# Performance work log

Measured on AMD Instinct MI355X. Metric: run time of the kernel, lower is better.

Reference implementation:

```python
import jax, jax.numpy as jnp
import numpy as np

N_NODES = 100000
N_EDGES = 1600000
IN_C, HID_C, OUT_C = 128, 128, 64


def setup_inputs() -> dict:
    key = jax.random.key(0)
    ks = jax.random.split(key, 5)
    x = jax.random.normal(ks[0], (N_NODES, IN_C), dtype=jnp.float32)
    edge_index = jax.random.randint(ks[1], (2, N_EDGES), 0, N_NODES, dtype=jnp.int32)
    W1 = jax.random.normal(ks[2], (IN_C, HID_C), dtype=jnp.float32) * (1.0 / np.sqrt(IN_C))
    W2 = jax.random.normal(ks[3], (HID_C, HID_C), dtype=jnp.float32) * (1.0 / np.sqrt(HID_C))
    W3 = jax.random.normal(ks[4], (HID_C, OUT_C), dtype=jnp.float32) * (1.0 / np.sqrt(HID_C))
    b1 = jnp.zeros((HID_C,), jnp.float32)
    b2 = jnp.zeros((HID_C,), jnp.float32)
    b3 = jnp.zeros((OUT_C,), jnp.float32)
    return {"x": x, "edge_index": edge_index, "W1": W1, "b1": b1,
            "W2": W2, "b2": b2, "W3": W3, "b3": b3}


def _gcn_norm(edge_index, num_nodes):
    # PyG gcn_norm: add self-loops, symmetric normalization D^-1/2 A D^-1/2
    loops = jnp.arange(num_nodes, dtype=edge_index.dtype)
    row = jnp.concatenate([edge_index[0], loops])  # source nodes
    col = jnp.concatenate([edge_index[1], loops])  # target nodes
    ones = jnp.ones(row.shape[0], jnp.float32)
    deg = jax.ops.segment_sum(ones, col, num_segments=num_nodes)
    dinv = jnp.where(deg > 0, jax.lax.rsqrt(deg), 0.0)
    norm = dinv[row] * dinv[col]  # [E + N]
    return row, col, norm


def _gcn_conv(h, row, col, norm, W, b, num_nodes):
    h = h @ W                                   # [N, out] dense transform first
    msg = h[row] * norm[:, None]                # gather + scale, [E+N, out]
    out = jax.ops.segment_sum(msg, col, num_segments=num_nodes)  # scatter-add
    return out + b


def reference(x, edge_index, W1, b1, W2, b2, W3, b3):
    n = x.shape[0]
    row, col, norm = _gcn_norm(edge_index, n)
    h = jax.nn.relu(_gcn_conv(x, row, col, norm, W1, b1, n))
    h = jax.nn.relu(_gcn_conv(h, row, col, norm, W2, b2, n))
    h = _gcn_conv(h, row, col, norm, W3, b3, n)
    return h
```

## Files before the change

kernel.cpp:

```cpp
#include <hip/hip_runtime.h>
#include <hip/hip_fp16.h>


#define K_DIM 128
#define CHUNK 8192
#define NBMAX 1024

typedef _Float16 f16x8 __attribute__((ext_vector_type(8)));
typedef float f32x4 __attribute__((ext_vector_type(4)));


__global__ __launch_bounds__(256) void hist_pass(const int* __restrict__ col, int E,
                                                 int NB, int B1, int* __restrict__ histG) {
    __shared__ int h[NBMAX];
    const int tid = threadIdx.x;
    for (int i = tid; i < NB; i += 256) h[i] = 0;
    __syncthreads();
    const int base = blockIdx.x * CHUNK;
    const int end = min(base + CHUNK, E);
    for (int e = base + tid; e < end; e += 256) atomicAdd(&h[col[e] >> 7], 1);
    __syncthreads();
    for (int i = tid; i < NB; i += 256) histG[(size_t)i * B1 + blockIdx.x] = h[i];
}

__global__ __launch_bounds__(256) void scan_blocks(int* __restrict__ data, int n,
                                                   int* __restrict__ bsum) {
    __shared__ int sh[256];
    const int tid = threadIdx.x;
    const int base = blockIdx.x * 1024;
    int v[4];
    int sum = 0;
#pragma unroll
    for (int j = 0; j < 4; ++j) {
        int i = base + tid * 4 + j;
        v[j] = (i < n) ? data[i] : 0;
        sum += v[j];
    }
    sh[tid] = sum;
    __syncthreads();
#pragma unroll
    for (int off = 1; off < 256; off <<= 1) {
        int t = (tid >= off) ? sh[tid - off] : 0;
        __syncthreads();
        sh[tid] += t;
        __syncthreads();
    }
    int run = (tid > 0) ? sh[tid - 1] : 0;
#pragma unroll
    for (int j = 0; j < 4; ++j) {
        int i = base + tid * 4 + j;
        if (i < n) data[i] = run;
        run += v[j];
    }
    if (tid == 255) bsum[blockIdx.x] = sh[255];
}

__global__ __launch_bounds__(256) void scan_single(int* __restrict__ data, int n) {
    __shared__ int sh[256];
    const int tid = threadIdx.x;
    int v[4];
    int sum = 0;
#pragma unroll
    for (int j = 0; j < 4; ++j) {
        int i = tid * 4 + j;
        v[j] = (i < n) ? data[i] : 0;
        sum += v[j];
    }
    sh[tid] = sum;
    __syncthreads();
#pragma unroll
    for (int off = 1; off < 256; off <<= 1) {
        int t = (tid >= off) ? sh[tid - off] : 0;
        __syncthreads();
        sh[tid] += t;
        __syncthreads();
    }
    int run = (tid > 0) ? sh[tid - 1] : 0;
#pragma unroll
    for (int j = 0; j < 4; ++j) {
        int i = tid * 4 + j;
        if (i < n) data[i] = run;
        run += v[j];
    }
}

__global__ void add_bsum(int* __restrict__ data, const int* __restrict__ bsum, int n) {
    int i = blockIdx.x * 256 + threadIdx.x;
    if (i < n) data[i] += bsum[i >> 10];
}

__global__ __launch_bounds__(256) void scatter_pass(const int* __restrict__ row,
                                                    const int* __restrict__ col, int E,
                                                    int NB, int B1,
                                                    const int* __restrict__ histG,
                                                    int* __restrict__ ebuf) {
    __shared__ int cur[NBMAX];
    const int tid = threadIdx.x;
    for (int i = tid; i < NB; i += 256) cur[i] = histG[(size_t)i * B1 + blockIdx.x];
    __syncthreads();
    const int base = blockIdx.x * CHUNK;
    const int end = min(base + CHUNK, E);
    for (int e = base + tid; e < end; e += 256) {
        int d = col[e];
        int s = row[e];
        int pos = atomicAdd(&cur[d >> 7], 1);
        ebuf[pos] = (s << 7) | (d & 127);
    }
}

__global__ __launch_bounds__(256) void build_csr(const int* __restrict__ ebuf,
                                                 const int* __restrict__ histG,
                                                 int NB, int B1, int N, int E,
                                                 int* __restrict__ offs,
                                                 float* __restrict__ dinv,
                                                 int* __restrict__ csr) {
    __shared__ int cnt[128];
    __shared__ int scn[128];
    __shared__ int curL[128];
    const int tid = threadIdx.x;
    const int b = blockIdx.x;
    const int S = histG[(size_t)b * B1];
    const int T = (b + 1 < NB) ? histG[(size_t)(b + 1) * B1] : E;

    if (tid < 128) cnt[tid] = 0;
    __syncthreads();
    for (int i = S + tid; i < T; i += 256) atomicAdd(&cnt[ebuf[i] & 127], 1);
    __syncthreads();
    if (tid < 128) scn[tid] = cnt[tid];
    __syncthreads();
#pragma unroll
    for (int off = 1; off < 128; off <<= 1) {
        int t = (tid < 128 && tid >= off) ? scn[tid - off] : 0;
        __syncthreads();
        if (tid < 128) scn[tid] += t;
        __syncthreads();
    }
    if (tid < 128) {
        int exc = (tid > 0) ? scn[tid - 1] : 0;
        int node = b * 128 + tid;
        if (node < N) {
            offs[node] = S + exc;
            dinv[node] = rsqrtf((float)(cnt[tid] + 1));
        }
        curL[tid] = S + exc;
    }
    if (b == 0 && tid == 0) offs[N] = E;
    __syncthreads();
    for (int i = S + tid; i < T; i += 256) {
        int p = ebuf[i];
        int pos = atomicAdd(&curL[p & 127], 1);
        csr[pos] = p >> 7;
    }
}


__global__ void cast_x(const float* __restrict__ x, __half* __restrict__ x16, int n8) {
    int i = blockIdx.x * 256 + threadIdx.x;
    if (i >= n8) return;
    float4 v0 = ((const float4*)x)[2 * i];
    float4 v1 = ((const float4*)x)[2 * i + 1];
    __half2 o[4] = {__float22half2_rn(make_float2(v0.x, v0.y)),
                    __float22half2_rn(make_float2(v0.z, v0.w)),
                    __float22half2_rn(make_float2(v1.x, v1.y)),
                    __float22half2_rn(make_float2(v1.z, v1.w))};
    ((float4*)x16)[i] = *(float4*)o;
}

__global__ void prep_wT(const float* __restrict__ W1, const float* __restrict__ W2,
                        const float* __restrict__ W3, __half* __restrict__ wT1,
                        __half* __restrict__ wT2, __half* __restrict__ wT3) {
    int tid = blockIdx.x * 256 + threadIdx.x;
    if (tid < 16384) {
        int n = tid >> 7, k = tid & 127;
        wT1[tid] = __float2half(W1[k * 128 + n]);
    } else if (tid < 32768) {
        int t = tid - 16384;
        int n = t >> 7, k = t & 127;
        wT2[t] = __float2half(W2[k * 128 + n]);
    } else if (tid < 40960) {
        int t = tid - 32768;
        int n = t >> 7, k = t & 127;
        wT3[t] = __float2half(W3[k * 64 + n]);
    }
}


template <int NCOLS>
__global__ __launch_bounds__(256) void gemm_f16(const __half* __restrict__ A,
                                                const __half* __restrict__ wT,
                                                const float* __restrict__ dinv,
                                                __half* __restrict__ out, int M) {
    constexpr int NT = NCOLS / 16;
    __shared__ __half sWT[NCOLS][136];

    const int tid = threadIdx.x;
    for (int idx = tid; idx < NCOLS * 16; idx += 256) {
        int n = idx >> 4, kc = (idx & 15) * 8;
        *(float4*)&sWT[n][kc] = *(const float4*)&wT[n * 128 + kc];
    }
    __syncthreads();

    const int wave = tid >> 6;
    const int l = tid & 63;
    const int lm = l & 15;
    const int kg = l >> 4;
    const int row0 = blockIdx.x * 128 + wave * 32;

    f32x4 acc[2][NT];
#pragma unroll
    for (int mt = 0; mt < 2; ++mt)
#pragma unroll
        for (int nt = 0; nt < NT; ++nt) acc[mt][nt] = {0.f, 0.f, 0.f, 0.f};

    const int m0 = row0 + lm;
    const int m1 = row0 + 16 + lm;
    const int mc0 = min(m0, M - 1);
    const int mc1 = min(m1, M - 1);

#pragma unroll
    for (int ks = 0; ks < 4; ++ks) {
        const int k0 = ks * 32 + kg * 8;
        f16x8 b0 = *(const f16x8*)&A[(size_t)mc0 * 128 + k0];
        f16x8 b1 = *(const f16x8*)&A[(size_t)mc1 * 128 + k0];
#pragma unroll
        for (int nt = 0; nt < NT; ++nt) {
            f16x8 a = *(const f16x8*)&sWT[nt * 16 + lm][k0];
            acc[0][nt] = __builtin_amdgcn_mfma_f32_16x16x32_f16(a, b0, acc[0][nt], 0, 0, 0);
            acc[1][nt] = __builtin_amdgcn_mfma_f32_16x16x32_f16(a, b1, acc[1][nt], 0, 0, 0);
        }
    }

#pragma unroll
    for (int mt = 0; mt < 2; ++mt) {
        const int m = (mt == 0) ? m0 : m1;
        if (m < M) {
            const float dv = dinv[m];
#pragma unroll
            for (int nt = 0; nt < NT; ++nt) {
                float z0 = acc[mt][nt][0] * dv, z1 = acc[mt][nt][1] * dv;
                float z2 = acc[mt][nt][2] * dv, z3 = acc[mt][nt][3] * dv;
                __half2 o[2] = {__float22half2_rn(make_float2(z0, z1)),
                                __float22half2_rn(make_float2(z2, z3))};
                *(float2*)&out[(size_t)m * NCOLS + nt * 16 + kg * 4] = *(float2*)o;
            }
        }
    }
}


template <bool RELU>
__global__ __launch_bounds__(256) void agg128(const __half* __restrict__ h,
                                              const float* __restrict__ dinv,
                                              const int* __restrict__ offs,
                                              const int* __restrict__ csr,
                                              const float* __restrict__ bias,
                                              __half* __restrict__ out, int N) {
    const int wid = (blockIdx.x * 256 + threadIdx.x) >> 6;
    if (wid >= N) return;
    const int l = threadIdx.x & 63;
    const int q = l >> 4;
    const int c = l & 15;
    const int beg = offs[wid], end = offs[wid + 1];
    const float di = dinv[wid];
    const float4* __restrict__ hp = (const float4*)h;

    float a[8] = {0.f, 0.f, 0.f, 0.f, 0.f, 0.f, 0.f, 0.f};
    if (beg < end) {
        const int last = end - 1;
        for (int e = beg; e < end; e += 8) {
            int i0 = e + q, i1 = e + 4 + q;
            float m0 = (i0 < end) ? 1.f : 0.f;
            float m1 = (i1 < end) ? 1.f : 0.f;
            int s0 = csr[min(i0, last)];
            int s1 = csr[min(i1, last)];
            float4 r0 = hp[(size_t)s0 * 16 + c];
            float4 r1 = hp[(size_t)s1 * 16 + c];
            const __half2* h0 = (const __half2*)&r0;
            const __half2* h1 = (const __half2*)&r1;
#pragma unroll
            for (int j = 0; j < 4; ++j) {
                float2 f0 = __half22float2(h0[j]);
                float2 f1 = __half22float2(h1[j]);
                a[2 * j] = fmaf(f0.x, m0, a[2 * j]);
                a[2 * j + 1] = fmaf(f0.y, m0, a[2 * j + 1]);
                a[2 * j] = fmaf(f1.x, m1, a[2 * j]);
                a[2 * j + 1] = fmaf(f1.y, m1, a[2 * j + 1]);
            }
        }
    }
#pragma unroll
    for (int j = 0; j < 8; ++j) {
        a[j] += __shfl_xor(a[j], 16);
        a[j] += __shfl_xor(a[j], 32);
    }
    {
        float4 rs = hp[(size_t)wid * 16 + c];
        const __half2* hs = (const __half2*)&rs;
#pragma unroll
        for (int j = 0; j < 4; ++j) {
            float2 f = __half22float2(hs[j]);
            a[2 * j] += f.x;
            a[2 * j + 1] += f.y;
        }
    }
    float4 b0 = ((const float4*)bias)[2 * c];
    float4 b1 = ((const float4*)bias)[2 * c + 1];
    float z[8];
    z[0] = fmaf(di, a[0], b0.x); z[1] = fmaf(di, a[1], b0.y);
    z[2] = fmaf(di, a[2], b0.z); z[3] = fmaf(di, a[3], b0.w);
    z[4] = fmaf(di, a[4], b1.x); z[5] = fmaf(di, a[5], b1.y);
    z[6] = fmaf(di, a[6], b1.z); z[7] = fmaf(di, a[7], b1.w);
    if (RELU) {
#pragma unroll
        for (int j = 0; j < 8; ++j) z[j] = fmaxf(z[j], 0.f);
    }
    if (q == 0) {
        __half2 o[4] = {__float22half2_rn(make_float2(z[0], z[1])),
                        __float22half2_rn(make_float2(z[2], z[3])),
                        __float22half2_rn(make_float2(z[4], z[5])),
                        __float22half2_rn(make_float2(z[6], z[7]))};
        ((float4*)out)[(size_t)wid * 16 + c] = *(float4*)o;
    }
}

__global__ __launch_bounds__(256) void agg64(const __half* __restrict__ h,
                                             const float* __restrict__ dinv,
                                             const int* __restrict__ offs,
                                             const int* __restrict__ csr,
                                             const float* __restrict__ bias,
                                             float* __restrict__ out, int N) {
    const int wid = (blockIdx.x * 256 + threadIdx.x) >> 6;
    if (wid >= N) return;
    const int l = threadIdx.x & 63;
    const int q = l >> 3;
    const int c = l & 7;
    const int beg = offs[wid], end = offs[wid + 1];
    const float di = dinv[wid];
    const float4* __restrict__ hp = (const float4*)h;

    float a[8] = {0.f, 0.f, 0.f, 0.f, 0.f, 0.f, 0.f, 0.f};
    if (beg < end) {
        const int last = end - 1;
        for (int e = beg; e < end; e += 8) {
            int i0 = e + q;
            float m0 = (i0 < end) ? 1.f : 0.f;
            int s0 = csr[min(i0, last)];
            float4 r0 = hp[(size_t)s0 * 8 + c];
            const __half2* h0 = (const __half2*)&r0;
#pragma unroll
            for (int j = 0; j < 4; ++j) {
                float2 f0 = __half22float2(h0[j]);
                a[2 * j] = fmaf(f0.x, m0, a[2 * j]);
                a[2 * j + 1] = fmaf(f0.y, m0, a[2 * j + 1]);
            }
        }
    }
#pragma unroll
    for (int j = 0; j < 8; ++j) {
        a[j] += __shfl_xor(a[j], 8);
        a[j] += __shfl_xor(a[j], 16);
        a[j] += __shfl_xor(a[j], 32);
    }
    {
        float4 rs = hp[(size_t)wid * 8 + c];
        const __half2* hs = (const __half2*)&rs;
#pragma unroll
        for (int j = 0; j < 4; ++j) {
            float2 f = __half22float2(hs[j]);
            a[2 * j] += f.x;
            a[2 * j + 1] += f.y;
        }
    }
    float4 b0 = ((const float4*)bias)[2 * c];
    float4 b1 = ((const float4*)bias)[2 * c + 1];
    float z[8];
    z[0] = fmaf(di, a[0], b0.x); z[1] = fmaf(di, a[1], b0.y);
    z[2] = fmaf(di, a[2], b0.z); z[3] = fmaf(di, a[3], b0.w);
    z[4] = fmaf(di, a[4], b1.x); z[5] = fmaf(di, a[5], b1.y);
    z[6] = fmaf(di, a[6], b1.z); z[7] = fmaf(di, a[7], b1.w);
    if (q == 0) {
        ((float4*)out)[(size_t)wid * 16 + 2 * c] = make_float4(z[0], z[1], z[2], z[3]);
        ((float4*)out)[(size_t)wid * 16 + 2 * c + 1] = make_float4(z[4], z[5], z[6], z[7]);
    }
}


extern "C" void kernel_launch(void* const* d_in, const int* in_sizes, int n_in,
                              void* d_out, int out_size, void* d_ws, size_t ws_size,
                              hipStream_t stream) {
    const float* x  = (const float*)d_in[0];
    const int*   ei = (const int*)d_in[1];
    const float* W1 = (const float*)d_in[2];
    const float* b1 = (const float*)d_in[3];
    const float* W2 = (const float*)d_in[4];
    const float* b2 = (const float*)d_in[5];
    const float* W3 = (const float*)d_in[6];
    const float* b3 = (const float*)d_in[7];

    const int N = in_sizes[0] / 128;
    const int E = in_sizes[1] / 2;
    const int* row = ei;
    const int* col = ei + E;

    const int NB = (N + 127) >> 7;
    const int B1 = (E + CHUNK - 1) / CHUNK;
    const int NBB1 = NB * B1;

    char* p = (char*)d_ws;
    auto alloc = [&](size_t bytes) {
        char* r = p;
        p += (bytes + 255) & ~(size_t)255;
        return r;
    };
    int*    offs  = (int*)alloc((size_t)(N + 1) * 4);
    float*  dinv  = (float*)alloc((size_t)N * 4);
    int*    histG = (int*)alloc((size_t)NBB1 * 4);
    int*    bsum  = (int*)alloc(1024 * 4);
    int*    ebuf  = (int*)alloc((size_t)E * 4);
    int*    csr   = (int*)alloc((size_t)E * 4);
    __half* bufA  = (__half*)alloc((size_t)N * 128 * 2);
    __half* bufB  = (__half*)alloc((size_t)N * 128 * 2);
    __half* wT1   = (__half*)alloc(16384 * 2);
    __half* wT2   = (__half*)alloc(16384 * 2);
    __half* wT3   = (__half*)alloc(8192 * 2);

    const int nsb = (NBB1 + 1023) / 1024;

    hist_pass<<<B1, 256, 0, stream>>>(col, E, NB, B1, histG);
    scan_blocks<<<nsb, 256, 0, stream>>>(histG, NBB1, bsum);
    scan_single<<<1, 256, 0, stream>>>(bsum, nsb);
    add_bsum<<<(NBB1 + 255) / 256, 256, 0, stream>>>(histG, bsum, NBB1);
    scatter_pass<<<B1, 256, 0, stream>>>(row, col, E, NB, B1, histG, ebuf);
    build_csr<<<NB, 256, 0, stream>>>(ebuf, histG, NB, B1, N, E, offs, dinv, csr);

    const int n8 = N * 128 / 8;
    cast_x<<<(n8 + 255) / 256, 256, 0, stream>>>(x, bufB, n8);
    prep_wT<<<160, 256, 0, stream>>>(W1, W2, W3, wT1, wT2, wT3);

    const int gGemm = (N + 127) / 128;
    const int gAgg = (N + 3) / 4;

    gemm_f16<128><<<gGemm, 256, 0, stream>>>(bufB, wT1, dinv, bufA, N);
    agg128<true><<<gAgg, 256, 0, stream>>>(bufA, dinv, offs, csr, b1, bufB, N);

    gemm_f16<128><<<gGemm, 256, 0, stream>>>(bufB, wT2, dinv, bufA, N);
    agg128<true><<<gAgg, 256, 0, stream>>>(bufA, dinv, offs, csr, b2, bufB, N);

    gemm_f16<64><<<gGemm, 256, 0, stream>>>(bufB, wT3, dinv, bufA, N);
    agg64<<<gAgg, 256, 0, stream>>>(bufA, dinv, offs, csr, b3, (float*)d_out, N);
}
```

Measured before the change: 286.1 us.

## Fuse aggregation with next-layer GEMM and fold fp32 cast into first GEMM

Folds the x fp32-to-fp16 conversion into the first GEMM, which now reads the fp32 input directly. Each aggregation layer now writes its 128-node tile to a swizzled LDS buffer, then runs the next layer's MFMA GEMM on that tile. This removes the cast kernel and the round trips of the intermediate activations through global memory. In exchange, each block now processes 128 nodes with one wave looping over 32 nodes, which cuts parallelism for the latency-bound gather. The 32KB LDS buffer limits occupancy, and weights are read from global memory instead of LDS.

After: 405.7 us. 41.8% more time.

```diff
diff --git a/kernel.cpp b/kernel.cpp
--- a/kernel.cpp
+++ b/kernel.cpp
@@ -151,19 +151,6 @@
         int pos = atomicAdd(&curL[p & 127], 1);
         csr[pos] = p >> 7;
     }
-}
-
-
-__global__ void cast_x(const float* __restrict__ x, __half* __restrict__ x16, int n8) {
-    int i = blockIdx.x * 256 + threadIdx.x;
-    if (i >= n8) return;
-    float4 v0 = ((const float4*)x)[2 * i];
-    float4 v1 = ((const float4*)x)[2 * i + 1];
-    __half2 o[4] = {__float22half2_rn(make_float2(v0.x, v0.y)),
-                    __float22half2_rn(make_float2(v0.z, v0.w)),
-                    __float22half2_rn(make_float2(v1.x, v1.y)),
-                    __float22half2_rn(make_float2(v1.z, v1.w))};
-    ((float4*)x16)[i] = *(float4*)o;
 }
 
 __global__ void prep_wT(const float* __restrict__ W1, const float* __restrict__ W2,
@@ -185,32 +172,22 @@
 }
 
 
-template <int NCOLS>
-__global__ __launch_bounds__(256) void gemm_f16(const __half* __restrict__ A,
-                                                const __half* __restrict__ wT,
-                                                const float* __restrict__ dinv,
-                                                __half* __restrict__ out, int M) {
-    constexpr int NT = NCOLS / 16;
-    __shared__ __half sWT[NCOLS][136];
-
-    const int tid = threadIdx.x;
-    for (int idx = tid; idx < NCOLS * 16; idx += 256) {
-        int n = idx >> 4, kc = (idx & 15) * 8;
-        *(float4*)&sWT[n][kc] = *(const float4*)&wT[n * 128 + kc];
-    }
-    __syncthreads();
-
+__global__ __launch_bounds__(256) void gemm_x(const float* __restrict__ X,
+                                              const __half* __restrict__ wT,
+                                              const float* __restrict__ dinv,
+                                              __half* __restrict__ out, int M) {
+    const int tid = threadIdx.x;
     const int wave = tid >> 6;
     const int l = tid & 63;
     const int lm = l & 15;
     const int kg = l >> 4;
     const int row0 = blockIdx.x * 128 + wave * 32;
 
-    f32x4 acc[2][NT];
+    f32x4 acc[2][8];
 #pragma unroll
     for (int mt = 0; mt < 2; ++mt)
 #pragma unroll
-        for (int nt = 0; nt < NT; ++nt) acc[mt][nt] = {0.f, 0.f, 0.f, 0.f};
+        for (int nt = 0; nt < 8; ++nt) acc[mt][nt] = {0.f, 0.f, 0.f, 0.f};
 
     const int m0 = row0 + lm;
     const int m1 = row0 + 16 + lm;
@@ -220,11 +197,17 @@
 #pragma unroll
     for (int ks = 0; ks < 4; ++ks) {
         const int k0 = ks * 32 + kg * 8;
-        f16x8 b0 = *(const f16x8*)&A[(size_t)mc0 * 128 + k0];
-        f16x8 b1 = *(const f16x8*)&A[(size_t)mc1 * 128 + k0];
-#pragma unroll
-        for (int nt = 0; nt < NT; ++nt) {
-            f16x8 a = *(const f16x8*)&sWT[nt * 16 + lm][k0];
+        float4 u0 = *(const float4*)&X[(size_t)mc0 * 128 + k0];
+        float4 u1 = *(const float4*)&X[(size_t)mc0 * 128 + k0 + 4];
+        float4 u2 = *(const float4*)&X[(size_t)mc1 * 128 + k0];
+        float4 u3 = *(const float4*)&X[(size_t)mc1 * 128 + k0 + 4];
+        f16x8 b0 = {(_Float16)u0.x, (_Float16)u0.y, (_Float16)u0.z, (_Float16)u0.w,
+                    (_Float16)u1.x, (_Float16)u1.y, (_Float16)u1.z, (_Float16)u1.w};
+        f16x8 b1 = {(_Float16)u2.x, (_Float16)u2.y, (_Float16)u2.z, (_Float16)u2.w,
+                    (_Float16)u3.x, (_Float16)u3.y, (_Float16)u3.z, (_Float16)u3.w};
+#pragma unroll
+        for (int nt = 0; nt < 8; ++nt) {
+            f16x8 a = *(const f16x8*)&wT[(size_t)(nt * 16 + lm) * 128 + k0];
             acc[0][nt] = __builtin_amdgcn_mfma_f32_16x16x32_f16(a, b0, acc[0][nt], 0, 0, 0);
             acc[1][nt] = __builtin_amdgcn_mfma_f32_16x16x32_f16(a, b1, acc[1][nt], 0, 0, 0);
         }
@@ -234,6 +217,142 @@
     for (int mt = 0; mt < 2; ++mt) {
         const int m = (mt == 0) ? m0 : m1;
         if (m < M) {
+            const float dv = dinv[m];
+#pragma unroll
+            for (int nt = 0; nt < 8; ++nt) {
+                float z0 = acc[mt][nt][0] * dv, z1 = acc[mt][nt][1] * dv;
+                float z2 = acc[mt][nt][2] * dv, z3 = acc[mt][nt][3] * dv;
+                __half2 o[2] = {__float22half2_rn(make_float2(z0, z1)),
+                                __float22half2_rn(make_float2(z2, z3))};
+                *(float2*)&out[(size_t)m * 128 + nt * 16 + kg * 4] = *(float2*)o;
+            }
+        }
+    }
+}
+
+
+template <int NCOLS, bool RELU>
+__global__ __launch_bounds__(256) void agg_gemm(const __half* __restrict__ h,
+                                                const float* __restrict__ dinv,
+                                                const int* __restrict__ offs,
+                                                const int* __restrict__ csr,
+                                                const float* __restrict__ bias,
+                                                const __half* __restrict__ wT,
+                                                __half* __restrict__ out,
+                                                int N) {
+    constexpr int NT = NCOLS / 16;
+    __shared__ __align__(16) __half sH[128 * 128];
+
+    const int tid = threadIdx.x;
+    const int wave = tid >> 6;
+    const int l = tid & 63;
+    const int q = l >> 4;
+    const int c = l & 15;
+    const float4* __restrict__ hp = (const float4*)h;
+
+    for (int it = 0; it < 32; ++it) {
+        const int lr = wave * 32 + it;
+        const int node = blockIdx.x * 128 + lr;
+        float a[8] = {0.f, 0.f, 0.f, 0.f, 0.f, 0.f, 0.f, 0.f};
+        float z[8];
+        bool valid = node < N;
+        if (valid) {
+            const int beg = offs[node], end = offs[node + 1];
+            const float di = dinv[node];
+            if (beg < end) {
+                const int last = end - 1;
+                for (int e = beg; e < end; e += 8) {
+                    int i0 = e + q, i1 = e + 4 + q;
+                    float m0 = (i0 < end) ? 1.f : 0.f;
+                    float m1 = (i1 < end) ? 1.f : 0.f;
+                    int s0 = csr[min(i0, last)];
+                    int s1 = csr[min(i1, last)];
+                    float4 r0 = hp[(size_t)s0 * 16 + c];
+                    float4 r1 = hp[(size_t)s1 * 16 + c];
+                    const __half2* h0 = (const __half2*)&r0;
+                    const __half2* h1 = (const __half2*)&r1;
+#pragma unroll
+                    for (int j = 0; j < 4; ++j) {
+                        float2 f0 = __half22float2(h0[j]);
+                        float2 f1 = __half22float2(h1[j]);
+                        a[2 * j] = fmaf(f0.x, m0, a[2 * j]);
+                        a[2 * j + 1] = fmaf(f0.y, m0, a[2 * j + 1]);
+                        a[2 * j] = fmaf(f1.x, m1, a[2 * j]);
+                        a[2 * j + 1] = fmaf(f1.y, m1, a[2 * j + 1]);
+                    }
+                }
+            }
+#pragma unroll
+            for (int j = 0; j < 8; ++j) {
+                a[j] += __shfl_xor(a[j], 16);
+                a[j] += __shfl_xor(a[j], 32);
+            }
+            {
+                float4 rs = hp[(size_t)node * 16 + c];
+                const __half2* hs = (const __half2*)&rs;
+#pragma unroll
+                for (int j = 0; j < 4; ++j) {
+                    float2 f = __half22float2(hs[j]);
+                    a[2 * j] += f.x;
+                    a[2 * j + 1] += f.y;
+                }
+            }
+            float4 b0 = ((const float4*)bias)[2 * c];
+            float4 b1 = ((const float4*)bias)[2 * c + 1];
+            z[0] = fmaf(di, a[0], b0.x); z[1] = fmaf(di, a[1], b0.y);
+            z[2] = fmaf(di, a[2], b0.z); z[3] = fmaf(di, a[3], b0.w);
+            z[4] = fmaf(di, a[4], b1.x); z[5] = fmaf(di, a[5], b1.y);
+            z[6] = fmaf(di, a[6], b1.z); z[7] = fmaf(di, a[7], b1.w);
+            if (RELU) {
+#pragma unroll
+                for (int j = 0; j < 8; ++j) z[j] = fmaxf(z[j], 0.f);
+            }
+        } else {
+#pragma unroll
+            for (int j = 0; j < 8; ++j) z[j] = 0.f;
+        }
+        if (q == 0) {
+            __half2 o[4] = {__float22half2_rn(make_float2(z[0], z[1])),
+                            __float22half2_rn(make_float2(z[2], z[3])),
+                            __float22half2_rn(make_float2(z[4], z[5])),
+                            __float22half2_rn(make_float2(z[6], z[7]))};
+            const int cc = c ^ (lr & 7);
+            *(float4*)&sH[lr * 128 + cc * 8] = *(float4*)o;
+        }
+    }
+    __syncthreads();
+
+    const int lm = l & 15;
+    const int kg = l >> 4;
+    const int row0 = blockIdx.x * 128 + wave * 32;
+
+    f32x4 acc[2][NT];
+#pragma unroll
+    for (int mt = 0; mt < 2; ++mt)
+#pragma unroll
+        for (int nt = 0; nt < NT; ++nt) acc[mt][nt] = {0.f, 0.f, 0.f, 0.f};
+
+    const int lr0 = wave * 32 + lm;
+    const int lr1 = wave * 32 + 16 + lm;
+
+#pragma unroll
+    for (int ks = 0; ks < 4; ++ks) {
+        const int k0 = ks * 32 + kg * 8;
+        const int ch = ks * 4 + kg;
+        f16x8 b0 = *(const f16x8*)&sH[lr0 * 128 + (ch ^ (lr0 & 7)) * 8];
+        f16x8 b1 = *(const f16x8*)&sH[lr1 * 128 + (ch ^ (lr1 & 7)) * 8];
+#pragma unroll
+        for (int nt = 0; nt < NT; ++nt) {
+            f16x8 a = *(const f16x8*)&wT[(size_t)(nt * 16 + lm) * 128 + k0];
+            acc[0][nt] = __builtin_amdgcn_mfma_f32_16x16x32_f16(a, b0, acc[0][nt], 0, 0, 0);
+            acc[1][nt] = __builtin_amdgcn_mfma_f32_16x16x32_f16(a, b1, acc[1][nt], 0, 0, 0);
+        }
+    }
+
+#pragma unroll
+    for (int mt = 0; mt < 2; ++mt) {
+        const int m = row0 + mt * 16 + lm;
+        if (m < N) {
             const float dv = dinv[m];
 #pragma unroll
             for (int nt = 0; nt < NT; ++nt) {
@@ -244,82 +363,6 @@
                 *(float2*)&out[(size_t)m * NCOLS + nt * 16 + kg * 4] = *(float2*)o;
             }
         }
-    }
-}
-
-
-template <bool RELU>
-__global__ __launch_bounds__(256) void agg128(const __half* __restrict__ h,
-                                              const float* __restrict__ dinv,
-                                              const int* __restrict__ offs,
-                                              const int* __restrict__ csr,
-                                              const float* __restrict__ bias,
-                                              __half* __restrict__ out, int N) {
-    const int wid = (blockIdx.x * 256 + threadIdx.x) >> 6;
-    if (wid >= N) return;
-    const int l = threadIdx.x & 63;
-    const int q = l >> 4;
-    const int c = l & 15;
-    const int beg = offs[wid], end = offs[wid + 1];
-    const float di = dinv[wid];
-    const float4* __restrict__ hp = (const float4*)h;
-
-    float a[8] = {0.f, 0.f, 0.f, 0.f, 0.f, 0.f, 0.f, 0.f};
-    if (beg < end) {
-        const int last = end - 1;
-        for (int e = beg; e < end; e += 8) {
-            int i0 = e + q, i1 = e + 4 + q;
-            float m0 = (i0 < end) ? 1.f : 0.f;
-            float m1 = (i1 < end) ? 1.f : 0.f;
-            int s0 = csr[min(i0, last)];
-            int s1 = csr[min(i1, last)];
-            float4 r0 = hp[(size_t)s0 * 16 + c];
-            float4 r1 = hp[(size_t)s1 * 16 + c];
-            const __half2* h0 = (const __half2*)&r0;
-            const __half2* h1 = (const __half2*)&r1;
-#pragma unroll
-            for (int j = 0; j < 4; ++j) {
-                float2 f0 = __half22float2(h0[j]);
-                float2 f1 = __half22float2(h1[j]);
-                a[2 * j] = fmaf(f0.x, m0, a[2 * j]);
-                a[2 * j + 1] = fmaf(f0.y, m0, a[2 * j + 1]);
-                a[2 * j] = fmaf(f1.x, m1, a[2 * j]);
-                a[2 * j + 1] = fmaf(f1.y, m1, a[2 * j + 1]);
-            }
-        }
-    }
-#pragma unroll
-    for (int j = 0; j < 8; ++j) {
-        a[j] += __shfl_xor(a[j], 16);
-        a[j] += __shfl_xor(a[j], 32);
-    }
-    {
-        float4 rs = hp[(size_t)wid * 16 + c];
-        const __half2* hs = (const __half2*)&rs;
-#pragma unroll
-        for (int j = 0; j < 4; ++j) {
-            float2 f = __half22float2(hs[j]);
-            a[2 * j] += f.x;
-            a[2 * j + 1] += f.y;
-        }
-    }
-    float4 b0 = ((const float4*)bias)[2 * c];
-    float4 b1 = ((const float4*)bias)[2 * c + 1];
-    float z[8];
-    z[0] = fmaf(di, a[0], b0.x); z[1] = fmaf(di, a[1], b0.y);
-    z[2] = fmaf(di, a[2], b0.z); z[3] = fmaf(di, a[3], b0.w);
-    z[4] = fmaf(di, a[4], b1.x); z[5] = fmaf(di, a[5], b1.y);
-    z[6] = fmaf(di, a[6], b1.z); z[7] = fmaf(di, a[7], b1.w);
-    if (RELU) {
-#pragma unroll
-        for (int j = 0; j < 8; ++j) z[j] = fmaxf(z[j], 0.f);
-    }
-    if (q == 0) {
-        __half2 o[4] = {__float22half2_rn(make_float2(z[0], z[1])),
-                        __float22half2_rn(make_float2(z[2], z[3])),
-                        __float22half2_rn(make_float2(z[4], z[5])),
-                        __float22half2_rn(make_float2(z[6], z[7]))};
-        ((float4*)out)[(size_t)wid * 16 + c] = *(float4*)o;
     }
 }
 
@@ -433,19 +476,13 @@
     scatter_pass<<<B1, 256, 0, stream>>>(row, col, E, NB, B1, histG, ebuf);
     build_csr<<<NB, 256, 0, stream>>>(ebuf, histG, NB, B1, N, E, offs, dinv, csr);
 
-    const int n8 = N * 128 / 8;
-    cast_x<<<(n8 + 255) / 256, 256, 0, stream>>>(x, bufB, n8);
     prep_wT<<<160, 256, 0, stream>>>(W1, W2, W3, wT1, wT2, wT3);
 
-    const int gGemm = (N + 127) / 128;
+    const int gTile = (N + 127) / 128;
     const int gAgg = (N + 3) / 4;
 
-    gemm_f16<128><<<gGemm, 256, 0, stream>>>(bufB, wT1, dinv, bufA, N);
-    agg128<true><<<gAgg, 256, 0, stream>>>(bufA, dinv, offs, csr, b1, bufB, N);
-
-    gemm_f16<128><<<gGemm, 256, 0, stream>>>(bufB, wT2, dinv, bufA, N);
-    agg128<true><<<gAgg, 256, 0, stream>>>(bufA, dinv, offs, csr, b2, bufB, N);
-
-    gemm_f16<64><<<gGemm, 256, 0, stream>>>(bufB, wT3, dinv, bufA, N);
+    gemm_x<<<gTile, 256, 0, stream>>>(x, wT1, dinv, bufA, N);
+    agg_gemm<128, true><<<gTile, 256, 0, stream>>>(bufA, dinv, offs, csr, b1, wT2, bufB, N);
+    agg_gemm<64, true><<<gTile, 256, 0, stream>>>(bufB, dinv, offs, csr, b2, wT3, bufA, N);
     agg64<<<gAgg, 256, 0, stream>>>(bufA, dinv, offs, csr, b3, (float*)d_out, N);
 }
```
